# Optimization experiments

Measured on AMD Instinct MI355X. Metric: run time of the kernel, lower is better.

Reference implementation:

```python
import jax, jax.numpy as jnp
import numpy as np

POOLED_H = 7
POOLED_W = 7
SPATIAL_SCALE = 0.25
S = 2  # sampling_ratio (static grid per bin)
ALIGNED_OFFSET = 0.5  # aligned=True


def setup_inputs() -> dict:
    key = jax.random.key(0)
    k1, k2, k3, k4 = jax.random.split(key, 4)
    B, C, H, W = 2, 256, 200, 200
    K = 1000
    x = jax.random.normal(k1, (B, C, H, W), dtype=jnp.float32)
    img_w = W / SPATIAL_SCALE  # 800.0, image-space coords
    img_h = H / SPATIAL_SCALE
    bidx = jax.random.randint(k2, (K,), 0, B).astype(jnp.float32)
    xy1 = jax.random.uniform(k3, (K, 2), dtype=jnp.float32) * jnp.array([img_w * 0.7, img_h * 0.7], jnp.float32)
    wh = jax.random.uniform(k4, (K, 2), dtype=jnp.float32) * jnp.array([img_w * 0.3, img_h * 0.3], jnp.float32) + 1.0
    rois = jnp.concatenate([bidx[:, None], xy1[:, 0:1], xy1[:, 1:2],
                            xy1[:, 0:1] + wh[:, 0:1], xy1[:, 1:2] + wh[:, 1:2]], axis=1)
    return {"x": x, "rois": rois}


def _axis(start, bin_size, pooled, limit):
    """Per-axis sample coords + bilinear corner indices/weights.
    start, bin_size: [K]. Returns low, high [K, pooled*S] int32 and
    w_low, w_high [K, pooled*S] float (validity folded into weights)."""
    p = jnp.arange(pooled, dtype=start.dtype)
    s = (jnp.arange(S, dtype=start.dtype) + 0.5) / S
    coord = start[:, None, None] + (p[None, :, None] + s[None, None, :]) * bin_size[:, None, None]
    coord = coord.reshape(coord.shape[0], pooled * S)  # [K, pooled*S]
    valid = ((coord >= -1.0) & (coord <= limit)).astype(coord.dtype)
    c = jnp.maximum(coord, 0.0)
    low0 = jnp.floor(c).astype(jnp.int32)
    cap = low0 >= limit - 1
    low = jnp.where(cap, limit - 1, low0)
    high = jnp.where(cap, limit - 1, low0 + 1)
    c = jnp.where(cap, low.astype(c.dtype), c)
    l = c - low.astype(c.dtype)
    h = 1.0 - l
    return low, high, h * valid, l * valid


def _roi_align(x, rois):
    B, C, H, W = x.shape
    bidx = rois[:, 0].astype(jnp.int32)
    start_w = rois[:, 1] * SPATIAL_SCALE - ALIGNED_OFFSET
    start_h = rois[:, 2] * SPATIAL_SCALE - ALIGNED_OFFSET
    end_w = rois[:, 3] * SPATIAL_SCALE - ALIGNED_OFFSET
    end_h = rois[:, 4] * SPATIAL_SCALE - ALIGNED_OFFSET
    bin_h = (end_h - start_h) / POOLED_H
    bin_w = (end_w - start_w) / POOLED_W
    yl, yh, wy0, wy1 = _axis(start_h, bin_h, POOLED_H, H)  # [K, PH*S]
    xl, xh, wx0, wx1 = _axis(start_w, bin_w, POOLED_W, W)  # [K, PW*S]
    xt = x.reshape(B, C, H * W).transpose(0, 2, 1)  # [B, HW, C]

    def gather(yi, xi):
        pos = yi[:, :, None] * W + xi[:, None, :]          # [K, NY, NX]
        return xt[bidx[:, None, None], pos, :]             # [K, NY, NX, C]

    out = (wy0[:, :, None, None] * wx0[:, None, :, None] * gather(yl, xl)
         + wy0[:, :, None, None] * wx1[:, None, :, None] * gather(yl, xh)
         + wy1[:, :, None, None] * wx0[:, None, :, None] * gather(yh, xl)
         + wy1[:, :, None, None] * wx1[:, None, :, None] * gather(yh, xh))
    K = rois.shape[0]
    # average over the SxS sample grid inside each bin
    out = out.reshape(K, POOLED_H, S, POOLED_W, S, C).sum(axis=(2, 4)) / float(S * S)
    return out.transpose(0, 3, 1, 2)  # [K, C, PH, PW]


def reference(x, rois):
    return _roi_align(x, rois)
```

## Files before the change

### kernel.cpp

```cpp
#include <hip/hip_runtime.h>
#include <hip/hip_bf16.h>


#define PH 7
#define PW 7
#define SCALE 0.25f
#define C_ 256
#define CH_ 128
#define H_ 200
#define W_ 200
#define HW_ (H_ * W_)

typedef float f32x4 __attribute__((ext_vector_type(4)));

__global__ void __launch_bounds__(512)
transpose_kernel(const float* __restrict__ x, __hip_bfloat16* __restrict__ xt) {
    __shared__ float tile[64][65];
    int hw0 = blockIdx.x * 64;
    int c0  = blockIdx.y * 64;
    int b   = blockIdx.z;
    int tx = threadIdx.x;
    int ty = threadIdx.y;
    const float* xb = x + (size_t)b * C_ * HW_;
#pragma unroll
    for (int j = 0; j < 8; ++j) {
        int cl = ty + 8 * j;
        tile[cl][tx] = __builtin_nontemporal_load(&xb[(size_t)(c0 + cl) * HW_ + hw0 + tx]);
    }
    __syncthreads();
    __hip_bfloat16* xtb = xt + (size_t)b * HW_ * C_;
#pragma unroll
    for (int j = 0; j < 8; ++j) {
        int rl = ty + 8 * j;
        float v = tile[tx][rl];
        xtb[(size_t)(hw0 + rl) * C_ + c0 + tx] = __float2bfloat16(v);
    }
}

__global__ void __launch_bounds__(512)
roi_main(const __hip_bfloat16* __restrict__ xt, const float* __restrict__ rois,
         float* __restrict__ out, int K) {
    __shared__ float s_out[CH_ * 49];
    __shared__ int   s_ylo[14], s_yhi[14], s_xlo[14], s_xhi[14];
    __shared__ float s_wy0[14], s_wy1[14], s_wx0[14], s_wx1[14];
    __shared__ int   s_b;

    int k     = blockIdx.x >> 1;
    int chalf = blockIdx.x & 1;
    int t = threadIdx.x;
    const float* r = rois + (size_t)k * 5;
    if (t == 0) s_b = (int)r[0];
    if (t < 28) {
        bool isy = t < 14;
        int i = isy ? t : t - 14;
        float start = (isy ? r[2] : r[1]) * SCALE - 0.5f;
        float end   = (isy ? r[4] : r[3]) * SCALE - 0.5f;
        float bin = (end - start) * (1.0f / 7.0f);
        int limit = isy ? H_ : W_;
        float pp   = (float)(i >> 1);
        float soff = (i & 1) ? 0.75f : 0.25f;
        float coord = fmaf(pp + soff, bin, start);
        float valid = (coord >= -1.0f && coord <= (float)limit) ? 1.0f : 0.0f;
        float cc = fmaxf(coord, 0.0f);
        int low0 = (int)floorf(cc);
        bool cap = low0 >= limit - 1;
        int lo = cap ? limit - 1 : low0;
        int hi = cap ? limit - 1 : low0 + 1;
        cc = cap ? (float)lo : cc;
        float l = cc - (float)lo;
        float w1 = l * valid, w0 = (1.0f - l) * valid;
        if (isy) { s_ylo[i] = lo; s_yhi[i] = hi; s_wy0[i] = w0; s_wy1[i] = w1; }
        else     { s_xlo[i] = lo; s_xhi[i] = hi; s_wx0[i] = w0; s_wx1[i] = w1; }
    }
    __syncthreads();

    int cg = t & 15;
    int pq = t >> 4;

    const __hip_bfloat16* xb = xt + (size_t)s_b * HW_ * C_ + chalf * CH_ + cg * 8;

    for (int p = pq; p < 49; p += 32) {
        int ph = p / 7;
        int pw = p - ph * 7;
        float acc[8];
#pragma unroll
        for (int j = 0; j < 8; ++j) acc[j] = 0.0f;

#pragma unroll
        for (int sy = 0; sy < 2; ++sy) {
            int ys = 2 * ph + sy;
            int yl = s_ylo[ys], yh = s_yhi[ys];
            float wy0 = s_wy0[ys], wy1 = s_wy1[ys];
#pragma unroll
            for (int sx = 0; sx < 2; ++sx) {
                int xs = 2 * pw + sx;
                int xl = s_xlo[xs], xh = s_xhi[xs];
                float wx0 = s_wx0[xs], wx1 = s_wx1[xs];
                float w00 = wy0 * wx0, w01 = wy0 * wx1;
                float w10 = wy1 * wx0, w11 = wy1 * wx1;
                uint4 v00 = *(const uint4*)(xb + ((size_t)(yl * W_ + xl) << 8));
                uint4 v01 = *(const uint4*)(xb + ((size_t)(yl * W_ + xh) << 8));
                uint4 v10 = *(const uint4*)(xb + ((size_t)(yh * W_ + xl) << 8));
                uint4 v11 = *(const uint4*)(xb + ((size_t)(yh * W_ + xh) << 8));
                const unsigned* a00 = (const unsigned*)&v00;
                const unsigned* a01 = (const unsigned*)&v01;
                const unsigned* a10 = (const unsigned*)&v10;
                const unsigned* a11 = (const unsigned*)&v11;
#pragma unroll
                for (int w = 0; w < 4; ++w) {
                    float f00l = __uint_as_float(a00[w] << 16);
                    float f00h = __uint_as_float(a00[w] & 0xffff0000u);
                    float f01l = __uint_as_float(a01[w] << 16);
                    float f01h = __uint_as_float(a01[w] & 0xffff0000u);
                    float f10l = __uint_as_float(a10[w] << 16);
                    float f10h = __uint_as_float(a10[w] & 0xffff0000u);
                    float f11l = __uint_as_float(a11[w] << 16);
                    float f11h = __uint_as_float(a11[w] & 0xffff0000u);
                    acc[2 * w]     = fmaf(w00, f00l, acc[2 * w]);
                    acc[2 * w]     = fmaf(w01, f01l, acc[2 * w]);
                    acc[2 * w]     = fmaf(w10, f10l, acc[2 * w]);
                    acc[2 * w]     = fmaf(w11, f11l, acc[2 * w]);
                    acc[2 * w + 1] = fmaf(w00, f00h, acc[2 * w + 1]);
                    acc[2 * w + 1] = fmaf(w01, f01h, acc[2 * w + 1]);
                    acc[2 * w + 1] = fmaf(w10, f10h, acc[2 * w + 1]);
                    acc[2 * w + 1] = fmaf(w11, f11h, acc[2 * w + 1]);
                }
            }
        }
#pragma unroll
        for (int j = 0; j < 8; ++j)
            s_out[(cg * 8 + j) * 49 + p] = acc[j] * 0.25f;
    }
    __syncthreads();

    const f32x4* sv = (const f32x4*)s_out;
    f32x4* ov = (f32x4*)(out + ((size_t)k * C_ + chalf * CH_) * 49);
    for (int i = t; i < (CH_ * 49) / 4; i += 512)
        __builtin_nontemporal_store(sv[i], &ov[i]);
}

__device__ __forceinline__ void axis_sample(float coord, int limit,
                                            int& lo, int& hi,
                                            float& w0, float& w1) {
    float fl = (float)limit;
    float valid = (coord >= -1.0f && coord <= fl) ? 1.0f : 0.0f;
    float c = fmaxf(coord, 0.0f);
    int low0 = (int)floorf(c);
    bool cap = low0 >= limit - 1;
    lo = cap ? limit - 1 : low0;
    hi = cap ? limit - 1 : low0 + 1;
    c = cap ? (float)lo : c;
    float l = c - (float)lo;
    w1 = l * valid;
    w0 = (1.0f - l) * valid;
}

__global__ void __launch_bounds__(256)
roi_align_fallback(const float* __restrict__ x, const float* __restrict__ rois,
                   float* __restrict__ out, int total) {
    int idx = blockIdx.x * blockDim.x + threadIdx.x;
    if (idx >= total) return;
    int pw = idx % PW;
    int ph = (idx / PW) % PH;
    int c  = (idx / (PW * PH)) % C_;
    int k  = idx / (PW * PH * C_);
    const float* r = rois + (size_t)k * 5;
    int b = (int)r[0];
    float start_w = r[1] * SCALE - 0.5f;
    float start_h = r[2] * SCALE - 0.5f;
    float bin_w = (r[3] * SCALE - 0.5f - start_w) / (float)PW;
    float bin_h = (r[4] * SCALE - 0.5f - start_h) / (float)PH;
    const float* xp = x + ((size_t)b * C_ + c) * (size_t)HW_;
    float acc = 0.0f;
#pragma unroll
    for (int sy = 0; sy < 2; ++sy) {
        float yc = start_h + ((float)ph + (sy + 0.5f) * 0.5f) * bin_h;
        int yl, yh; float wy0, wy1;
        axis_sample(yc, H_, yl, yh, wy0, wy1);
        const float* row0 = xp + (size_t)yl * W_;
        const float* row1 = xp + (size_t)yh * W_;
#pragma unroll
        for (int sx = 0; sx < 2; ++sx) {
            float xc = start_w + ((float)pw + (sx + 0.5f) * 0.5f) * bin_w;
            int xl, xh; float wx0, wx1;
            axis_sample(xc, W_, xl, xh, wx0, wx1);
            acc += wy0 * (wx0 * row0[xl] + wx1 * row0[xh])
                 + wy1 * (wx0 * row1[xl] + wx1 * row1[xh]);
        }
    }
    out[idx] = acc * 0.25f;
}

extern "C" void kernel_launch(void* const* d_in, const int* in_sizes, int n_in,
                              void* d_out, int out_size, void* d_ws, size_t ws_size,
                              hipStream_t stream) {
    const float* x    = (const float*)d_in[0];
    const float* rois = (const float*)d_in[1];
    float* out = (float*)d_out;
    int K = in_sizes[1] / 5;

    size_t need = (size_t)2 * HW_ * C_ * sizeof(__hip_bfloat16);
    if (ws_size >= need) {
        __hip_bfloat16* xt = (__hip_bfloat16*)d_ws;
        dim3 tgrid(HW_ / 64, C_ / 64, 2);
        dim3 tblock(64, 8);
        transpose_kernel<<<tgrid, tblock, 0, stream>>>(x, xt);
        roi_main<<<K * 2, 512, 0, stream>>>(xt, rois, out, K);
    } else {
        int total = K * C_ * PH * PW;
        roi_align_fallback<<<(total + 255) / 256, 256, 0, stream>>>(x, rois, out, total);
    }
}
```

Before: 62.70 us.

## Sort ROIs by batch and y-center and remap blocks per XCD for cache locality

Adds a single-block bitonic sort that orders ROIs by batch index and quantized vertical center, producing a permutation that roi_main uses to choose which ROI each block handles. Block IDs are also remapped so that consecutive logical ROIs land on the same XCD, which is meant to raise L2 hit rates for overlapping feature-map regions. The cost is an extra serial kernel launch with many syncthreads, run alongside the transpose, plus one indirect lookup per block.

```diff
diff --git a/kernel.cpp b/kernel.cpp
--- a/kernel.cpp
+++ b/kernel.cpp
@@ -37,16 +37,56 @@
     }
 }
 
+__global__ void __launch_bounds__(1024)
+sort_rois_kernel(const float* __restrict__ rois, int K, int* __restrict__ perm) {
+    __shared__ int s[1024];
+    int t = threadIdx.x;
+    int key;
+    if (t < K) {
+        const float* r = rois + (size_t)t * 5;
+        int b = (int)r[0];
+        float yc = (r[2] + r[4]) * (0.5f * SCALE);
+        int yq = min(max((int)yc, 0), 511);
+        key = ((b * 512 + yq) << 12) | t;
+    } else {
+        key = 0x7FFFFFFF;
+    }
+    s[t] = key;
+    __syncthreads();
+    for (int k2 = 2; k2 <= 1024; k2 <<= 1) {
+        for (int j = k2 >> 1; j > 0; j >>= 1) {
+            int ixj = t ^ j;
+            if (ixj > t) {
+                int a = s[t], bv = s[ixj];
+                bool up = ((t & k2) == 0);
+                if ((a > bv) == up) { s[t] = bv; s[ixj] = a; }
+            }
+            __syncthreads();
+        }
+    }
+    if (t < K) perm[t] = s[t] & 0xFFF;
+}
+
+__global__ void identity_perm_kernel(int K, int* __restrict__ perm) {
+    int i = blockIdx.x * blockDim.x + threadIdx.x;
+    if (i < K) perm[i] = i;
+}
+
 __global__ void __launch_bounds__(512)
 roi_main(const __hip_bfloat16* __restrict__ xt, const float* __restrict__ rois,
-         float* __restrict__ out, int K) {
+         const int* __restrict__ perm, float* __restrict__ out, int K) {
     __shared__ float s_out[CH_ * 49];
     __shared__ int   s_ylo[14], s_yhi[14], s_xlo[14], s_xhi[14];
     __shared__ float s_wy0[14], s_wy1[14], s_wx0[14], s_wx1[14];
     __shared__ int   s_b;
 
-    int k     = blockIdx.x >> 1;
-    int chalf = blockIdx.x & 1;
+    int nwg = gridDim.x;
+    int q = nwg >> 3, rr = nwg & 7;
+    int xcd = blockIdx.x & 7, pos = blockIdx.x >> 3;
+    int logical = (xcd < rr ? xcd * (q + 1) : rr * (q + 1) + (xcd - rr) * q) + pos;
+
+    int k     = perm[logical >> 1];
+    int chalf = logical & 1;
     int t = threadIdx.x;
     const float* r = rois + (size_t)k * 5;
     if (t == 0) s_b = (int)r[0];
@@ -199,13 +239,19 @@
     float* out = (float*)d_out;
     int K = in_sizes[1] / 5;
 
-    size_t need = (size_t)2 * HW_ * C_ * sizeof(__hip_bfloat16);
-    if (ws_size >= need) {
+    size_t xtbytes = (size_t)2 * HW_ * C_ * sizeof(__hip_bfloat16);
+    size_t need = xtbytes + 4096 * sizeof(int);
+    if (ws_size >= need && K <= 4096) {
         __hip_bfloat16* xt = (__hip_bfloat16*)d_ws;
+        int* perm = (int*)((char*)d_ws + xtbytes);
         dim3 tgrid(HW_ / 64, C_ / 64, 2);
         dim3 tblock(64, 8);
         transpose_kernel<<<tgrid, tblock, 0, stream>>>(x, xt);
-        roi_main<<<K * 2, 512, 0, stream>>>(xt, rois, out, K);
+        if (K <= 1024)
+            sort_rois_kernel<<<1, 1024, 0, stream>>>(rois, K, perm);
+        else
+            identity_perm_kernel<<<(K + 255) / 256, 256, 0, stream>>>(K, perm);
+        roi_main<<<K * 2, 512, 0, stream>>>(xt, rois, perm, out, K);
     } else {
         int total = K * C_ * PH * PW;
         roi_align_fallback<<<(total + 255) / 256, 256, 0, stream>>>(x, rois, out, total);
```

After: 59.97 us. -4.4%, faster.
